# Kernel optimization log

Hardware: AMD Instinct MI355X
Metric: run time of the kernel (lower is better)

## Reference

```python
import jax, jax.numpy as jnp
import numpy as np

NUM_HEADS = 16
EPS = 1e-6
NEG_INF = -1e9


def layer_norm(x, scale, bias):
    m = jnp.mean(x, axis=-1, keepdims=True)
    v = jnp.mean(jnp.square(x - m), axis=-1, keepdims=True)
    return (x - m) * jax.lax.rsqrt(v + EPS) * scale + bias


def mha(x_q, x_kv, wq, wk, wv, wo, causal):
    B, Sq, D = x_q.shape
    Sk = x_kv.shape[1]
    H = NUM_HEADS
    Dh = D // H
    q = (x_q @ wq).reshape(B, Sq, H, Dh) * (1.0 / np.sqrt(Dh))
    k = (x_kv @ wk).reshape(B, Sk, H, Dh)
    v = (x_kv @ wv).reshape(B, Sk, H, Dh)
    scores = jnp.einsum('bqhf,bkhf->bhqk', q, k)  # [B,H,Sq,Sk]
    if causal:
        mask = jnp.tril(jnp.ones((Sq, Sk), dtype=bool))
        scores = jnp.where(mask, scores, NEG_INF)
    p = jax.nn.softmax(scores, axis=-1)
    o = jnp.einsum('bhqk,bkhf->bqhf', p, v).reshape(B, Sq, D)
    return o @ wo


def setup_inputs() -> dict:
    key = jax.random.key(0)
    ks = jax.random.split(key, 12)
    B, S, D, F = 2, 2048, 1024, 4096
    w = 0.02
    return {
        'targets': jax.random.normal(ks[0], (B, S, D), jnp.float32),
        'encoded': jax.random.normal(ks[1], (B, S, D), jnp.float32),
        'ln1_s': jnp.ones((D,), jnp.float32),
        'ln1_b': jnp.zeros((D,), jnp.float32),
        'sa_wq': jax.random.normal(ks[2], (D, D), jnp.float32) * w,
        'sa_wk': jax.random.normal(ks[3], (D, D), jnp.float32) * w,
        'sa_wv': jax.random.normal(ks[4], (D, D), jnp.float32) * w,
        'sa_wo': jax.random.normal(ks[5], (D, D), jnp.float32) * w,
        'ln2_s': jnp.ones((D,), jnp.float32),
        'ln2_b': jnp.zeros((D,), jnp.float32),
        'ca_wq': jax.random.normal(ks[6], (D, D), jnp.float32) * w,
        'ca_wk': jax.random.normal(ks[7], (D, D), jnp.float32) * w,
        'ca_wv': jax.random.normal(ks[8], (D, D), jnp.float32) * w,
        'ca_wo': jax.random.normal(ks[9], (D, D), jnp.float32) * w,
        'ln3_s': jnp.ones((D,), jnp.float32),
        'ln3_b': jnp.zeros((D,), jnp.float32),
        'mlp_w1': jax.random.normal(ks[10], (D, F), jnp.float32) * w,
        'mlp_b1': jnp.zeros((F,), jnp.float32),
        'mlp_w2': jax.random.normal(ks[11], (F, D), jnp.float32) * w,
        'mlp_b2': jnp.zeros((D,), jnp.float32),
    }


def reference(targets, encoded, ln1_s, ln1_b, sa_wq, sa_wk, sa_wv, sa_wo,
              ln2_s, ln2_b, ca_wq, ca_wk, ca_wv, ca_wo,
              ln3_s, ln3_b, mlp_w1, mlp_b1, mlp_w2, mlp_b2):
    # Pre-LN causal self-attention + residual
    x = layer_norm(targets, ln1_s, ln1_b)
    x = mha(x, x, sa_wq, sa_wk, sa_wv, sa_wo, causal=True)
    x = x + targets
    # Pre-LN cross-attention over encoder output + residual
    y = layer_norm(x, ln2_s, ln2_b)
    y = mha(y, encoded, ca_wq, ca_wk, ca_wv, ca_wo, causal=False)
    y = y + x
    # Pre-LN MLP + residual
    z = layer_norm(y, ln3_s, ln3_b)
    z = jax.nn.relu(z @ mlp_w1 + mlp_b1) @ mlp_w2 + mlp_b2
    return y + z
```

## Files before the change

### kernel.cpp

```cpp
#include <hip/hip_runtime.h>


#define DEV __device__ __forceinline__

typedef __attribute__((ext_vector_type(8))) _Float16 half8;
typedef __attribute__((ext_vector_type(4))) _Float16 half4;
typedef __attribute__((ext_vector_type(2))) _Float16 half2v;
typedef __attribute__((ext_vector_type(4))) float    f32x4;

#define GLB(p) ((const __attribute__((address_space(1))) void*)(p))
#define LDS(p) ((__attribute__((address_space(3))) void*)(p))

DEV half2v pk(float a, float b) {
  return __builtin_bit_cast(half2v, __builtin_amdgcn_cvt_pkrtz(a, b));
}
DEV half4 pk4(float a, float b, float c, float d) {
  half2v lo = pk(a, b), hi = pk(c, d);
  half4 r; r.x = lo.x; r.y = lo.y; r.z = hi.x; r.w = hi.y;
  return r;
}

DEV float wave_sum_f(float v) {
  #pragma unroll
  for (int off = 32; off; off >>= 1) v += __shfl_xor(v, off);
  return v;
}

struct WtArgs { const float* w[8]; _Float16* wt[8]; };

__global__ __launch_bounds__(256) void wt_square(WtArgs a) {
  const float* w = a.w[blockIdx.z];
  _Float16* wt = a.wt[blockIdx.z];
  __shared__ float t[32][33];
  const int tx = threadIdx.x, ty = threadIdx.y;
  const int n0 = blockIdx.x * 32, k0 = blockIdx.y * 32;
  #pragma unroll
  for (int i = ty; i < 32; i += 8)
    t[i][tx] = w[(size_t)(k0 + i) * 1024 + n0 + tx];
  __syncthreads();
  #pragma unroll
  for (int i = ty; i < 32; i += 8)
    wt[(size_t)(n0 + i) * 1024 + k0 + tx] = (_Float16)t[tx][i];
}

__global__ __launch_bounds__(256) void wt_one(const float* __restrict__ w,
                                              _Float16* __restrict__ wt,
                                              int K, int N) {
  __shared__ float t[32][33];
  const int tx = threadIdx.x, ty = threadIdx.y;
  const int n0 = blockIdx.x * 32, k0 = blockIdx.y * 32;
  #pragma unroll
  for (int i = ty; i < 32; i += 8)
    t[i][tx] = w[(size_t)(k0 + i) * N + n0 + tx];
  __syncthreads();
  #pragma unroll
  for (int i = ty; i < 32; i += 8)
    wt[(size_t)(n0 + i) * K + k0 + tx] = (_Float16)t[tx][i];
}

__global__ __launch_bounds__(256) void cvt_f16(const float* __restrict__ in,
                                               _Float16* __restrict__ out) {
  const size_t i = ((size_t)blockIdx.x * 256 + threadIdx.x) * 4;
  const float4 v = *(const float4*)(in + i);
  *(half4*)(out + i) = pk4(v.x, v.y, v.z, v.w);
}

__global__ __launch_bounds__(256) void ln_kernel(const float* __restrict__ x,
                                                 const float* __restrict__ sc,
                                                 const float* __restrict__ bi,
                                                 _Float16* __restrict__ out) {
  const int row = blockIdx.x;
  const int t = threadIdx.x;
  const float4 v = ((const float4*)(x + (size_t)row * 1024))[t];
  float s  = v.x + v.y + v.z + v.w;
  float s2 = v.x * v.x + v.y * v.y + v.z * v.z + v.w * v.w;
  s = wave_sum_f(s); s2 = wave_sum_f(s2);
  __shared__ float red[8];
  const int lane = t & 63, wid = t >> 6;
  if (lane == 0) { red[wid] = s; red[4 + wid] = s2; }
  __syncthreads();
  s  = red[0] + red[1] + red[2] + red[3];
  s2 = red[4] + red[5] + red[6] + red[7];
  const float mean = s * (1.f / 1024.f);
  const float rstd = rsqrtf(s2 * (1.f / 1024.f) - mean * mean + 1e-6f);
  const float4 sv = ((const float4*)sc)[t];
  const float4 bv = ((const float4*)bi)[t];
  half4 o = pk4((v.x - mean) * rstd * sv.x + bv.x,
                (v.y - mean) * rstd * sv.y + bv.y,
                (v.z - mean) * rstd * sv.z + bv.z,
                (v.w - mean) * rstd * sv.w + bv.w);
  ((half4*)(out + (size_t)row * 1024))[t] = o;
}

template <int EPI, int BM, int BN, int BK>
__global__ __launch_bounds__(256)
void gemm_f16(const _Float16* __restrict__ A, const _Float16* __restrict__ Bt,
              void* __restrict__ Cout, const float* __restrict__ bias,
              const float* __restrict__ resid, int M, int N, int K,
              float scl, int sclCols, _Float16* __restrict__ vt, int vcol0) {
  constexpr int AM = BM / 32;
  constexpr int AN = BN / 32;
  constexpr int RA = BM * BK / 2048;
  constexpr int RB = BN * BK / 2048;
  constexpr int TPR = BK / 8;
  constexpr int RPR = 2048 / BK;
  __shared__ _Float16 As[2][BM * BK];
  __shared__ _Float16 Bs[2][BN * BK];
  const int tid = threadIdx.x;
  const int lane = tid & 63, wid = tid >> 6;
  const int wm = wid >> 1, wn = wid & 1;
  const int q = lane >> 4, m15 = lane & 15;
  const int bm = blockIdx.y, bn = blockIdx.x;

  const int trow = tid / TPR;
  const int tcol = (tid % TPR) * 8;
  const _Float16* Ab = A + ((size_t)bm * BM + trow) * K + tcol;
  const _Float16* Bb = Bt + ((size_t)bn * BN + trow) * K + tcol;

  f32x4 acc[AM][AN] = {};

  auto stage = [&](int k0, int buf) {
    #pragma unroll
    for (int r = 0; r < RA; r++)
      __builtin_amdgcn_global_load_lds(GLB(Ab + (size_t)r * RPR * K + k0),
                                       LDS(&As[buf][r * 2048 + wid * 512]), 16, 0, 0);
    #pragma unroll
    for (int r = 0; r < RB; r++)
      __builtin_amdgcn_global_load_lds(GLB(Bb + (size_t)r * RPR * K + k0),
                                       LDS(&Bs[buf][r * 2048 + wid * 512]), 16, 0, 0);
  };

  stage(0, 0);
  const int nit = K / BK;
  for (int it = 0; it < nit; it++) {
    const int buf = it & 1;
    __syncthreads();
    if (it + 1 < nit) stage((it + 1) * BK, buf ^ 1);
    #pragma unroll
    for (int kk = 0; kk < BK / 32; kk++) {
      half8 af[AM], bf[AN];
      #pragma unroll
      for (int i = 0; i < AM; i++)
        af[i] = *(const half8*)&As[buf][(wm * (BM / 2) + i * 16 + m15) * BK + kk * 32 + q * 8];
      #pragma unroll
      for (int i = 0; i < AN; i++)
        bf[i] = *(const half8*)&Bs[buf][(wn * (BN / 2) + i * 16 + m15) * BK + kk * 32 + q * 8];
      #pragma unroll
      for (int mi = 0; mi < AM; mi++)
        #pragma unroll
        for (int ni = 0; ni < AN; ni++)
          acc[mi][ni] = __builtin_amdgcn_mfma_f32_16x16x32_f16(af[mi], bf[ni],
                                                               acc[mi][ni], 0, 0, 0);
    }
  }

  const int rowbase = bm * BM + wm * (BM / 2);
  const int colbase = bn * BN + wn * (BN / 2);
  #pragma unroll
  for (int ni = 0; ni < AN; ni++) {
    const int col = colbase + ni * 16 + m15;
    float bv = 0.f;
    if (EPI == 2 || EPI == 4) bv = bias[col];
    const float cs = (EPI == 1 || EPI == 5) ? (col < sclCols ? scl : 1.f) : 1.f;
    if (EPI == 5 && col >= vcol0) {
      const int d = col & 63, hh = (col >> 6) & 15;
      #pragma unroll
      for (int mi = 0; mi < AM; mi++) {
        const int row = rowbase + mi * 16 + q * 4;
        const int bb = row >> 11, ss = row & 2047;
        half4 ov = pk4(acc[mi][ni][0], acc[mi][ni][1],
                       acc[mi][ni][2], acc[mi][ni][3]);
        *(half4*)(vt + ((size_t)(bb * 16 + hh) * 64 + d) * 2048 + ss) = ov;
      }
      continue;
    }
    #pragma unroll
    for (int mi = 0; mi < AM; mi++) {
      #pragma unroll
      for (int r = 0; r < 4; r++) {
        const int row = rowbase + mi * 16 + q * 4 + r;
        const size_t idx = (size_t)row * N + col;
        float v = acc[mi][ni][r];
        if (EPI == 1 || EPI == 5) {
          ((_Float16*)Cout)[idx] = (_Float16)(v * cs);
        } else if (EPI == 2) {
          v += bv; v = v > 0.f ? v : 0.f;
          ((_Float16*)Cout)[idx] = (_Float16)v;
        } else if (EPI == 3) {
          ((float*)Cout)[idx] = v + resid[idx];
        } else {
          ((float*)Cout)[idx] = v + bv + resid[idx];
        }
      }
    }
  }
}

__global__ __launch_bounds__(256, 4)
void flash_attn(const _Float16* __restrict__ Q, int qs,
                const _Float16* __restrict__ Kp, int ks,
                const _Float16* __restrict__ Vt,
                _Float16* __restrict__ Opart, float* __restrict__ Lpart,
                int S, int Sk, int causal) {
  __shared__ _Float16 Ks[64 * 72];
  __shared__ _Float16 Vs[64 * 72];
  __shared__ _Float16 Pq[4][32 * 72];
  const int tid = threadIdx.x;
  const int lane = tid & 63, wid = tid >> 6;
  const int quad = lane >> 4, c15 = lane & 15;

  const int gx = gridDim.x;
  const int lid = blockIdx.x + gx * (blockIdx.y + 16 * blockIdx.z);
  const int xcd = lid & 7, slot = lid >> 3;
  const int bh = xcd * 4 + (slot / gx);
  const int qs2 = slot % gx;
  const int h = bh & 15, b = bh >> 4;
  int qb = qs2 >> 1;
  const int split = qs2 & 1;
  const int NQB = gx >> 1;
  if (causal) qb = (qb & 1) ? (NQB - 1 - (qb >> 1)) : (qb >> 1);
  const int qw0 = qb * 128 + wid * 32;

  half8 qf[2][2];
  #pragma unroll
  for (int nt = 0; nt < 2; nt++)
    #pragma unroll
    for (int kk = 0; kk < 2; kk++)
      qf[nt][kk] = *(const half8*)(Q + (size_t)(b * S + qw0 + nt * 16 + c15) * qs +
                                   h * 64 + kk * 32 + quad * 8);

  f32x4 oacc[4][2];
  #pragma unroll
  for (int i = 0; i < 4; i++)
    #pragma unroll
    for (int j = 0; j < 2; j++)
      oacc[i][j] = (f32x4){0.f, 0.f, 0.f, 0.f};
  float lpart[2] = {0.f, 0.f};

  const int ntF = causal ? (2 * qb + 2) : (Sk >> 6);
  const _Float16* Kg = Kp + (size_t)b * Sk * ks + h * 64;
  const _Float16* Vg = Vt + (size_t)(b * 16 + h) * 64 * Sk;

  const int srow = tid >> 3, sg8 = (tid & 7) * 8;
  half8 rk[2], rv[2];
  auto ldkv = [&](int jb) {
    #pragma unroll
    for (int i = 0; i < 2; i++) {
      rk[i] = *(const half8*)(Kg + (size_t)(jb + srow + i * 32) * ks + sg8);
      rv[i] = *(const half8*)(Vg + (size_t)(srow + i * 32) * Sk + jb + sg8);
    }
  };
  ldkv(split * 64);

  for (int t = split; t < ntF; t += 2) {
    const int jb = t << 6;
    __syncthreads();
    #pragma unroll
    for (int i = 0; i < 2; i++) {
      *(half8*)&Ks[(srow + i * 32) * 72 + sg8] = rk[i];
      *(half8*)&Vs[(srow + i * 32) * 72 + sg8] = rv[i];
    }
    __syncthreads();
    if (t + 2 < ntF) ldkv(jb + 128);

    if (causal && jb > qw0 + 31) continue;

    f32x4 s[4][2];
    #pragma unroll
    for (int mt = 0; mt < 4; mt++) {
      const half8 kf0 = *(const half8*)&Ks[(mt * 16 + c15) * 72 + quad * 8];
      const half8 kf1 = *(const half8*)&Ks[(mt * 16 + c15) * 72 + 32 + quad * 8];
      #pragma unroll
      for (int nt = 0; nt < 2; nt++) {
        f32x4 z = {0.f, 0.f, 0.f, 0.f};
        z = __builtin_amdgcn_mfma_f32_16x16x32_f16(kf0, qf[nt][0], z, 0, 0, 0);
        z = __builtin_amdgcn_mfma_f32_16x16x32_f16(kf1, qf[nt][1], z, 0, 0, 0);
        s[mt][nt] = z;
      }
    }

    if (causal && jb + 63 > qw0) {
      #pragma unroll
      for (int mt = 0; mt < 4; mt++)
        #pragma unroll
        for (int nt = 0; nt < 2; nt++) {
          const int qglob = qw0 + nt * 16 + c15;
          #pragma unroll
          for (int rr = 0; rr < 4; rr++) {
            const int kglob = jb + mt * 16 + quad * 4 + rr;
            if (kglob > qglob) s[mt][nt][rr] = -1e30f;
          }
        }
    }

    #pragma unroll
    for (int nt = 0; nt < 2; nt++) {
      float psum = 0.f;
      #pragma unroll
      for (int mt = 0; mt < 4; mt++) {
        #pragma unroll
        for (int rr = 0; rr < 4; rr++) {
          const float p = exp2f(s[mt][nt][rr]);
          s[mt][nt][rr] = p;
          psum += p;
        }
      }
      lpart[nt] += psum;
      #pragma unroll
      for (int mtk = 0; mtk < 4; mtk++) {
        *(half4*)&Pq[wid][(nt * 16 + c15) * 72 + mtk * 16 + quad * 4] =
            pk4(s[mtk][nt][0], s[mtk][nt][1], s[mtk][nt][2], s[mtk][nt][3]);
      }
    }

    half8 pb[2][2];
    #pragma unroll
    for (int kk = 0; kk < 2; kk++)
      #pragma unroll
      for (int nt = 0; nt < 2; nt++)
        pb[kk][nt] = *(const half8*)&Pq[wid][(nt * 16 + c15) * 72 + kk * 32 + quad * 8];
    #pragma unroll
    for (int mtd = 0; mtd < 4; mtd++) {
      const half8 vf0 = *(const half8*)&Vs[(mtd * 16 + c15) * 72 + quad * 8];
      const half8 vf1 = *(const half8*)&Vs[(mtd * 16 + c15) * 72 + 32 + quad * 8];
      #pragma unroll
      for (int nt = 0; nt < 2; nt++) {
        oacc[mtd][nt] = __builtin_amdgcn_mfma_f32_16x16x32_f16(vf0, pb[0][nt],
                                                               oacc[mtd][nt], 0, 0, 0);
        oacc[mtd][nt] = __builtin_amdgcn_mfma_f32_16x16x32_f16(vf1, pb[1][nt],
                                                               oacc[mtd][nt], 0, 0, 0);
      }
    }
  }

  _Float16* Ob = Opart + (size_t)split * ((size_t)2 * S * 1024) +
                 (size_t)b * S * 1024;
  #pragma unroll
  for (int nt = 0; nt < 2; nt++) {
    float l = lpart[nt];
    l += __shfl_xor(l, 16);
    l += __shfl_xor(l, 32);
    const int qrow = qw0 + nt * 16 + c15;
    if (quad == 0)
      Lpart[((size_t)(split * 2 + b) * 16 + h) * S + qrow] = l;
    #pragma unroll
    for (int mtd = 0; mtd < 4; mtd++) {
      half4 ov = pk4(oacc[mtd][nt][0], oacc[mtd][nt][1],
                     oacc[mtd][nt][2], oacc[mtd][nt][3]);
      *(half4*)(Ob + (size_t)qrow * 1024 + h * 64 + mtd * 16 + quad * 4) = ov;
    }
  }
}

__global__ __launch_bounds__(256)
void attn_combine(const _Float16* __restrict__ Op, const float* __restrict__ Lp,
                  _Float16* __restrict__ O) {
  const int row = blockIdx.x, tid = threadIdx.x;
  const int col = tid << 2, h = tid >> 4;
  const int b = row >> 11, sq = row & 2047;
  const float la = Lp[((size_t)(b * 16 + h)) * 2048 + sq];
  const float lb = Lp[((size_t)((b + 2) * 16 + h)) * 2048 + sq];
  const float linv = 1.f / (la + lb);
  const half4 pa = *(const half4*)(Op + (size_t)row * 1024 + col);
  const half4 pb = *(const half4*)(Op + ((size_t)4096 + row) * 1024 + col);
  half4 o = pk4(((float)pa.x + (float)pb.x) * linv,
                ((float)pa.y + (float)pb.y) * linv,
                ((float)pa.z + (float)pb.z) * linv,
                ((float)pa.w + (float)pb.w) * linv);
  *(half4*)(O + (size_t)row * 1024 + col) = o;
}

extern "C" void kernel_launch(void* const* d_in, const int* in_sizes, int n_in,
                              void* d_out, int out_size, void* d_ws, size_t ws_size,
                              hipStream_t stream) {
  const float* targets = (const float*)d_in[0];
  const float* encoded = (const float*)d_in[1];
  const float* ln1_s = (const float*)d_in[2];
  const float* ln1_b = (const float*)d_in[3];
  const float* sa_wq = (const float*)d_in[4];
  const float* sa_wk = (const float*)d_in[5];
  const float* sa_wv = (const float*)d_in[6];
  const float* sa_wo = (const float*)d_in[7];
  const float* ln2_s = (const float*)d_in[8];
  const float* ln2_b = (const float*)d_in[9];
  const float* ca_wq = (const float*)d_in[10];
  const float* ca_wk = (const float*)d_in[11];
  const float* ca_wv = (const float*)d_in[12];
  const float* ca_wo = (const float*)d_in[13];
  const float* ln3_s = (const float*)d_in[14];
  const float* ln3_b = (const float*)d_in[15];
  const float* mlp_w1 = (const float*)d_in[16];
  const float* mlp_b1 = (const float*)d_in[17];
  const float* mlp_w2 = (const float*)d_in[18];
  const float* mlp_b2 = (const float*)d_in[19];

  const int B = 2, S = 2048, D = 1024, F = 4096, M = B * S;
  const size_t MB = 1024ull * 1024ull;
  const float QSCALE = 0.125f * 1.44269504f;
  char* ws = (char*)d_ws;
  _Float16* wsq   = (_Float16*)(ws);
  _Float16* w1t   = (_Float16*)(ws + 16 * MB);
  _Float16* w2t   = (_Float16*)(ws + 24 * MB);
  _Float16* Abf   = (_Float16*)(ws + 32 * MB);
  _Float16* encbf = (_Float16*)(ws + 40 * MB);
  _Float16* QKV   = (_Float16*)(ws + 48 * MB);
  _Float16* Qcb   = (_Float16*)(ws + 48 * MB);
  _Float16* KVb   = (_Float16*)(ws + 56 * MB);
  _Float16* h1    = (_Float16*)(ws + 48 * MB);
  float*    Lbuf  = (float*)(ws + 72 * MB);
  _Float16* Vtb   = (_Float16*)(ws + 80 * MB);
  _Float16* Aob   = (_Float16*)(ws + 88 * MB);
  float*    xres  = (float*)(ws + 96 * MB);
  float*    yres  = (float*)(ws + 112 * MB);
  _Float16* Opart = (_Float16*)(ws + 112 * MB);

  {
    WtArgs wa;
    const float* sw[8] = {sa_wq, sa_wk, sa_wv, sa_wo, ca_wq, ca_wk, ca_wv, ca_wo};
    for (int i = 0; i < 8; i++) { wa.w[i] = sw[i]; wa.wt[i] = wsq + (size_t)i * D * D; }
    wt_square<<<dim3(32, 32, 8), dim3(32, 8), 0, stream>>>(wa);
  }
  wt_one<<<dim3(F / 32, D / 32), dim3(32, 8), 0, stream>>>(mlp_w1, w1t, D, F);
  wt_one<<<dim3(D / 32, F / 32), dim3(32, 8), 0, stream>>>(mlp_w2, w2t, F, D);
  cvt_f16<<<(M * D) / 1024, 256, 0, stream>>>(encoded, encbf);

  const dim3 gA(2 * (S / 128), 16, B);

  ln_kernel<<<M, 256, 0, stream>>>(targets, ln1_s, ln1_b, Abf);
  gemm_f16<5, 128, 128, 32><<<dim3(3072 / 128, M / 128), 256, 0, stream>>>(
      Abf, wsq, QKV, nullptr, nullptr, M, 3072, D, QSCALE, 1024, Vtb, 2048);
  flash_attn<<<gA, 256, 0, stream>>>(QKV, 3072, QKV + 1024, 3072, Vtb,
                                     Opart, Lbuf, S, S, 1);
  attn_combine<<<M, 256, 0, stream>>>(Opart, Lbuf, Aob);
  gemm_f16<3, 128, 64, 64><<<dim3(1024 / 64, M / 128), 256, 0, stream>>>(
      Aob, wsq + 3ull * D * D, xres, nullptr, targets, M, D, D, 1.f, 0, nullptr, 0);

  ln_kernel<<<M, 256, 0, stream>>>(xres, ln2_s, ln2_b, Abf);
  gemm_f16<1, 128, 64, 64><<<dim3(1024 / 64, M / 128), 256, 0, stream>>>(
      Abf, wsq + 4ull * D * D, Qcb, nullptr, nullptr, M, D, D, QSCALE, 1024, nullptr, 0);
  gemm_f16<5, 64, 128, 32><<<dim3(2048 / 128, M / 64), 256, 0, stream>>>(
      encbf, wsq + 5ull * D * D, KVb, nullptr, nullptr, M, 2048, D, 1.f, 0, Vtb, 1024);
  flash_attn<<<gA, 256, 0, stream>>>(Qcb, 1024, KVb, 2048, Vtb,
                                     Opart, Lbuf, S, S, 0);
  attn_combine<<<M, 256, 0, stream>>>(Opart, Lbuf, Aob);
  gemm_f16<3, 128, 64, 64><<<dim3(1024 / 64, M / 128), 256, 0, stream>>>(
      Aob, wsq + 7ull * D * D, yres, nullptr, xres, M, D, D, 1.f, 0, nullptr, 0);

  ln_kernel<<<M, 256, 0, stream>>>(yres, ln3_s, ln3_b, Abf);
  gemm_f16<2, 128, 128, 32><<<dim3(F / 128, M / 128), 256, 0, stream>>>(
      Abf, w1t, h1, mlp_b1, nullptr, M, F, D, 1.f, 0, nullptr, 0);
  gemm_f16<4, 128, 64, 64><<<dim3(1024 / 64, M / 128), 256, 0, stream>>>(
      h1, w2t, (float*)d_out, mlp_b2, yres, M, D, F, 1.f, 0, nullptr, 0);

  (void)in_sizes; (void)n_in; (void)out_size; (void)ws_size;
}
```

Before: 609.6 us.

## Double-buffer flash-attention K/V via direct LDS loads; shuffle P in registers

The flash attention kernel now stages K and V tiles straight from global memory into double-buffered, XOR-swizzled LDS with global_load_lds, dropping the register round trip and one barrier per iteration. The P matrix is rearranged into MFMA operand layout with cross-lane shuffles instead of a per-wave LDS scratch, which removes LDS writes and reads. Separately, the N=1024 GEMMs (out-projections, cross-attn Q, MLP down) switch to 64-row tiles to launch more blocks. The risks are shuffle overhead, swizzle correctness, and smaller GEMM tiles giving less data reuse.

```diff
diff --git a/kernel.cpp b/kernel.cpp
--- a/kernel.cpp
+++ b/kernel.cpp
@@ -7,6 +7,7 @@
 typedef __attribute__((ext_vector_type(4))) _Float16 half4;
 typedef __attribute__((ext_vector_type(2))) _Float16 half2v;
 typedef __attribute__((ext_vector_type(4))) float    f32x4;
+typedef __attribute__((ext_vector_type(4))) unsigned int uint4v;
 
 #define GLB(p) ((const __attribute__((address_space(1))) void*)(p))
 #define LDS(p) ((__attribute__((address_space(3))) void*)(p))
@@ -202,9 +203,8 @@
                 const _Float16* __restrict__ Vt,
                 _Float16* __restrict__ Opart, float* __restrict__ Lpart,
                 int S, int Sk, int causal) {
-  __shared__ _Float16 Ks[64 * 72];
-  __shared__ _Float16 Vs[64 * 72];
-  __shared__ _Float16 Pq[4][32 * 72];
+  __shared__ _Float16 Ks[2][64 * 64];
+  __shared__ _Float16 Vs[2][64 * 64];
   const int tid = threadIdx.x;
   const int lane = tid & 63, wid = tid >> 6;
   const int quad = lane >> 4, c15 = lane & 15;
@@ -241,96 +241,116 @@
   const _Float16* Kg = Kp + (size_t)b * Sk * ks + h * 64;
   const _Float16* Vg = Vt + (size_t)(b * 16 + h) * 64 * Sk;
 
-  const int srow = tid >> 3, sg8 = (tid & 7) * 8;
-  half8 rk[2], rv[2];
-  auto ldkv = [&](int jb) {
-    #pragma unroll
-    for (int i = 0; i < 2; i++) {
-      rk[i] = *(const half8*)(Kg + (size_t)(jb + srow + i * 32) * ks + sg8);
-      rv[i] = *(const half8*)(Vg + (size_t)(srow + i * 32) * Sk + jb + sg8);
+  const int srow8 = lane >> 3;
+  const int ssw = (((lane & 7) ^ srow8) << 3);
+  auto stage = [&](int jb, int buf) {
+    #pragma unroll
+    for (int r = 0; r < 2; r++) {
+      const int row = wid * 8 + srow8 + r * 32;
+      __builtin_amdgcn_global_load_lds(
+          GLB(Kg + (size_t)(jb + row) * ks + ssw),
+          LDS(&Ks[buf][(wid * 8 + r * 32) * 64]), 16, 0, 0);
+      __builtin_amdgcn_global_load_lds(
+          GLB(Vg + (size_t)row * Sk + jb + ssw),
+          LDS(&Vs[buf][(wid * 8 + r * 32) * 64]), 16, 0, 0);
     }
   };
-  ldkv(split * 64);
-
-  for (int t = split; t < ntF; t += 2) {
+
+  const int t0 = split;
+  stage(t0 << 6, 0);
+  __syncthreads();
+
+  const int rsw = c15 & 7;
+  const int ck0 = ((quad ^ rsw) << 3);
+  const int ck1 = (((quad ^ 4) ^ rsw) << 3);
+
+  int cur = 0;
+  for (int t = t0; t < ntF; t += 2) {
     const int jb = t << 6;
-    __syncthreads();
-    #pragma unroll
-    for (int i = 0; i < 2; i++) {
-      *(half8*)&Ks[(srow + i * 32) * 72 + sg8] = rk[i];
-      *(half8*)&Vs[(srow + i * 32) * 72 + sg8] = rv[i];
-    }
-    __syncthreads();
-    if (t + 2 < ntF) ldkv(jb + 128);
-
-    if (causal && jb > qw0 + 31) continue;
-
-    f32x4 s[4][2];
-    #pragma unroll
-    for (int mt = 0; mt < 4; mt++) {
-      const half8 kf0 = *(const half8*)&Ks[(mt * 16 + c15) * 72 + quad * 8];
-      const half8 kf1 = *(const half8*)&Ks[(mt * 16 + c15) * 72 + 32 + quad * 8];
+    if (t + 2 < ntF) stage((t + 2) << 6, cur ^ 1);
+
+    if (!(causal && jb > qw0 + 31)) {
+      f32x4 s[4][2];
+      #pragma unroll
+      for (int mt = 0; mt < 4; mt++) {
+        const half8 kf0 = *(const half8*)&Ks[cur][(mt * 16 + c15) * 64 + ck0];
+        const half8 kf1 = *(const half8*)&Ks[cur][(mt * 16 + c15) * 64 + ck1];
+        #pragma unroll
+        for (int nt = 0; nt < 2; nt++) {
+          f32x4 z = {0.f, 0.f, 0.f, 0.f};
+          z = __builtin_amdgcn_mfma_f32_16x16x32_f16(kf0, qf[nt][0], z, 0, 0, 0);
+          z = __builtin_amdgcn_mfma_f32_16x16x32_f16(kf1, qf[nt][1], z, 0, 0, 0);
+          s[mt][nt] = z;
+        }
+      }
+
+      if (causal && jb + 63 > qw0) {
+        #pragma unroll
+        for (int mt = 0; mt < 4; mt++)
+          #pragma unroll
+          for (int nt = 0; nt < 2; nt++) {
+            const int qglob = qw0 + nt * 16 + c15;
+            #pragma unroll
+            for (int rr = 0; rr < 4; rr++) {
+              const int kglob = jb + mt * 16 + quad * 4 + rr;
+              if (kglob > qglob) s[mt][nt][rr] = -1e30f;
+            }
+          }
+      }
+
+      unsigned int pkd[4][2][2];
       #pragma unroll
       for (int nt = 0; nt < 2; nt++) {
-        f32x4 z = {0.f, 0.f, 0.f, 0.f};
-        z = __builtin_amdgcn_mfma_f32_16x16x32_f16(kf0, qf[nt][0], z, 0, 0, 0);
-        z = __builtin_amdgcn_mfma_f32_16x16x32_f16(kf1, qf[nt][1], z, 0, 0, 0);
-        s[mt][nt] = z;
-      }
-    }
-
-    if (causal && jb + 63 > qw0) {
-      #pragma unroll
-      for (int mt = 0; mt < 4; mt++)
-        #pragma unroll
-        for (int nt = 0; nt < 2; nt++) {
-          const int qglob = qw0 + nt * 16 + c15;
+        float psum = 0.f;
+        #pragma unroll
+        for (int mt = 0; mt < 4; mt++) {
           #pragma unroll
           for (int rr = 0; rr < 4; rr++) {
-            const int kglob = jb + mt * 16 + quad * 4 + rr;
-            if (kglob > qglob) s[mt][nt][rr] = -1e30f;
+            const float p = exp2f(s[mt][nt][rr]);
+            s[mt][nt][rr] = p;
+            psum += p;
           }
+          pkd[mt][nt][0] = __builtin_bit_cast(unsigned int,
+                             pk(s[mt][nt][0], s[mt][nt][1]));
+          pkd[mt][nt][1] = __builtin_bit_cast(unsigned int,
+                             pk(s[mt][nt][2], s[mt][nt][3]));
         }
-    }
-
-    #pragma unroll
-    for (int nt = 0; nt < 2; nt++) {
-      float psum = 0.f;
-      #pragma unroll
-      for (int mt = 0; mt < 4; mt++) {
-        #pragma unroll
-        for (int rr = 0; rr < 4; rr++) {
-          const float p = exp2f(s[mt][nt][rr]);
-          s[mt][nt][rr] = p;
-          psum += p;
+        lpart[nt] += psum;
+      }
+
+      half8 pb[2][2];
+      #pragma unroll
+      for (int kk = 0; kk < 2; kk++)
+        #pragma unroll
+        for (int nt = 0; nt < 2; nt++) {
+          unsigned int w[4];
+          #pragma unroll
+          for (int jd = 0; jd < 4; jd++) {
+            const int src = ((quad & 1) * 2 + (jd >> 1)) * 16 + c15;
+            const unsigned int xs = __shfl(pkd[2 * kk][nt][jd & 1], src);
+            const unsigned int ys = __shfl(pkd[2 * kk + 1][nt][jd & 1], src);
+            w[jd] = (quad & 2) ? ys : xs;
+          }
+          uint4v u = {w[0], w[1], w[2], w[3]};
+          pb[kk][nt] = __builtin_bit_cast(half8, u);
         }
-      }
-      lpart[nt] += psum;
-      #pragma unroll
-      for (int mtk = 0; mtk < 4; mtk++) {
-        *(half4*)&Pq[wid][(nt * 16 + c15) * 72 + mtk * 16 + quad * 4] =
-            pk4(s[mtk][nt][0], s[mtk][nt][1], s[mtk][nt][2], s[mtk][nt][3]);
-      }
-    }
-
-    half8 pb[2][2];
-    #pragma unroll
-    for (int kk = 0; kk < 2; kk++)
-      #pragma unroll
-      for (int nt = 0; nt < 2; nt++)
-        pb[kk][nt] = *(const half8*)&Pq[wid][(nt * 16 + c15) * 72 + kk * 32 + quad * 8];
-    #pragma unroll
-    for (int mtd = 0; mtd < 4; mtd++) {
-      const half8 vf0 = *(const half8*)&Vs[(mtd * 16 + c15) * 72 + quad * 8];
-      const half8 vf1 = *(const half8*)&Vs[(mtd * 16 + c15) * 72 + 32 + quad * 8];
-      #pragma unroll
-      for (int nt = 0; nt < 2; nt++) {
-        oacc[mtd][nt] = __builtin_amdgcn_mfma_f32_16x16x32_f16(vf0, pb[0][nt],
-                                                               oacc[mtd][nt], 0, 0, 0);
-        oacc[mtd][nt] = __builtin_amdgcn_mfma_f32_16x16x32_f16(vf1, pb[1][nt],
-                                                               oacc[mtd][nt], 0, 0, 0);
-      }
-    }
+
+      #pragma unroll
+      for (int mtd = 0; mtd < 4; mtd++) {
+        const half8 vf0 = *(const half8*)&Vs[cur][(mtd * 16 + c15) * 64 + ck0];
+        const half8 vf1 = *(const half8*)&Vs[cur][(mtd * 16 + c15) * 64 + ck1];
+        #pragma unroll
+        for (int nt = 0; nt < 2; nt++) {
+          oacc[mtd][nt] = __builtin_amdgcn_mfma_f32_16x16x32_f16(vf0, pb[0][nt],
+                                                                 oacc[mtd][nt], 0, 0, 0);
+          oacc[mtd][nt] = __builtin_amdgcn_mfma_f32_16x16x32_f16(vf1, pb[1][nt],
+                                                                 oacc[mtd][nt], 0, 0, 0);
+        }
+      }
+    }
+
+    __syncthreads();
+    cur ^= 1;
   }
 
   _Float16* Ob = Opart + (size_t)split * ((size_t)2 * S * 1024) +
@@ -432,24 +452,24 @@
   flash_attn<<<gA, 256, 0, stream>>>(QKV, 3072, QKV + 1024, 3072, Vtb,
                                      Opart, Lbuf, S, S, 1);
   attn_combine<<<M, 256, 0, stream>>>(Opart, Lbuf, Aob);
-  gemm_f16<3, 128, 64, 64><<<dim3(1024 / 64, M / 128), 256, 0, stream>>>(
+  gemm_f16<3, 64, 64, 64><<<dim3(1024 / 64, M / 64), 256, 0, stream>>>(
       Aob, wsq + 3ull * D * D, xres, nullptr, targets, M, D, D, 1.f, 0, nullptr, 0);
 
   ln_kernel<<<M, 256, 0, stream>>>(xres, ln2_s, ln2_b, Abf);
-  gemm_f16<1, 128, 64, 64><<<dim3(1024 / 64, M / 128), 256, 0, stream>>>(
+  gemm_f16<1, 64, 64, 64><<<dim3(1024 / 64, M / 64), 256, 0, stream>>>(
       Abf, wsq + 4ull * D * D, Qcb, nullptr, nullptr, M, D, D, QSCALE, 1024, nullptr, 0);
   gemm_f16<5, 64, 128, 32><<<dim3(2048 / 128, M / 64), 256, 0, stream>>>(
       encbf, wsq + 5ull * D * D, KVb, nullptr, nullptr, M, 2048, D, 1.f, 0, Vtb, 1024);
   flash_attn<<<gA, 256, 0, stream>>>(Qcb, 1024, KVb, 2048, Vtb,
                                      Opart, Lbuf, S, S, 0);
   attn_combine<<<M, 256, 0, stream>>>(Opart, Lbuf, Aob);
-  gemm_f16<3, 128, 64, 64><<<dim3(1024 / 64, M / 128), 256, 0, stream>>>(
+  gemm_f16<3, 64, 64, 64><<<dim3(1024 / 64, M / 64), 256, 0, stream>>>(
       Aob, wsq + 7ull * D * D, yres, nullptr, xres, M, D, D, 1.f, 0, nullptr, 0);
 
   ln_kernel<<<M, 256, 0, stream>>>(yres, ln3_s, ln3_b, Abf);
   gemm_f16<2, 128, 128, 32><<<dim3(F / 128, M / 128), 256, 0, stream>>>(
       Abf, w1t, h1, mlp_b1, nullptr, M, F, D, 1.f, 0, nullptr, 0);
-  gemm_f16<4, 128, 64, 64><<<dim3(1024 / 64, M / 128), 256, 0, stream>>>(
+  gemm_f16<4, 64, 64, 64><<<dim3(1024 / 64, M / 64), 256, 0, stream>>>(
       h1, w2t, (float*)d_out, mlp_b2, yres, M, D, F, 1.f, 0, nullptr, 0);
 
   (void)in_sizes; (void)n_in; (void)out_size; (void)ws_size;
```

Result: faster. 581.4 us (-4.6%).
